# Kernel optimization log

Hardware: AMD Instinct MI355X
Metric: run time of the kernel (lower is better)

## Reference

```python
import jax, jax.numpy as jnp
import numpy as np

N_ITER = 2          # GenSP n_iter
M_COEF = 0.0        # GenSP M (positional-feature weight)
AFF_SOFTMAX = 1.0   # GenSP affinity_softmax


def setup_inputs() -> dict:
    key = jax.random.key(0)
    x = jax.random.normal(key, (2, 64, 256, 256), dtype=jnp.float32)
    return {"x": x, "stoken_size": 16}


def reference(x, stoken_size):
    # Faithful JAX version of GenSP.forward / ssn_iter (softmax_order='v0',
    # ws=None -> ws=2*stride0-1, i.e. each pixel searches its 9 neighboring
    # superpixel centroids; dist_type='l2' squared distance).
    B, C, H, W = x.shape
    s = int(stoken_size)
    nH, nW = (H - 1) // s + 1, (W - 1) // s + 1
    nS = nH * nW
    N = H * W

    # append_grid: concat scaled (y,x) coordinate channels, scale = M/stride0
    scale = jnp.asarray(M_COEF / s, x.dtype)
    gy, gx = jnp.meshgrid(jnp.arange(H, dtype=x.dtype) * scale,
                          jnp.arange(W, dtype=x.dtype) * scale, indexing='ij')
    grid = jnp.broadcast_to(jnp.stack([gy, gx])[None], (B, 2, H, W))
    feats = jnp.concatenate([x, grid], axis=1)          # [B, C+2, H, W]
    C2 = C + 2
    pf = feats.reshape(B, C2, N)                        # pixel features

    # calc_init_centroid: adaptive_avg_pool2d to (nH, nW); H,W divisible by s
    cent = feats.reshape(B, C2, nH, s, nW, s).mean(axis=(3, 5)).reshape(B, C2, nS)

    # per-pixel base superpixel cell and its 3x3 candidate neighborhood
    yy, xx = jnp.meshgrid(jnp.arange(H), jnp.arange(W), indexing='ij')
    sy = (yy // s).reshape(-1)                          # [N]
    sx = (xx // s).reshape(-1)
    dy, dx = jnp.meshgrid(jnp.arange(-1, 2), jnp.arange(-1, 2), indexing='ij')
    dy = dy.reshape(-1); dx = dx.reshape(-1)            # [9]
    cy = sy[:, None] + dy[None]                         # [N, 9]
    cx = sx[:, None] + dx[None]
    valid = (cy >= 0) & (cy < nH) & (cx >= 0) & (cx < nW)
    cand = jnp.where(valid, cy * nW + cx, 0)            # candidate spixel ids
    pix = jnp.broadcast_to(jnp.arange(N)[:, None], (N, 9))
    flat = (cand * N + pix).reshape(-1)                 # [9N] flat COO index
    NEG = jnp.asarray(-1e30, x.dtype)

    affinity = None
    for it in range(N_ITER):
        ck = cent[:, :, cand]                           # [B, C2, N, 9] gather
        d = jnp.sum((pf[:, :, :, None] - ck) ** 2, axis=1)  # squared-l2 [B,N,9]
        logits = jnp.where(valid[None], -AFF_SOFTMAX * d, NEG)
        w = jax.nn.softmax(logits, axis=-1)             # softmax_order 'v0'
        w = jnp.where(valid[None], w, jnp.asarray(0.0, x.dtype))
        # sparse-COO -> dense scatter: A[b, spix, pix] = w
        A = jnp.zeros((B, nS * N), x.dtype).at[:, flat].add(w.reshape(B, -1))
        affinity = A.reshape(B, nS, N)
        if it < N_ITER - 1:
            # spixel_features = bmm(A, pf^T) / (A.sum(2) + 1e-16)
            num = jnp.einsum('bsn,bcn->bcs', affinity, pf)
            den = affinity.sum(axis=2)[:, None] + 1e-16
            cent = num / den
    return affinity
```

## Files before the change

### kernel.cpp

```cpp
#include <hip/hip_runtime.h>
#include <cstdint>


__device__ __forceinline__ unsigned short f2bf(float f) {
    unsigned u = __float_as_uint(f);
    u = (u + 0x7FFFu + ((u >> 16) & 1u)) >> 16;
    return (unsigned short)u;
}
__device__ __forceinline__ float bf2f(unsigned short h) {
    return __uint_as_float(((unsigned)h) << 16);
}

__global__ __launch_bounds__(256) void kcent0(const float* __restrict__ x,
                                              float* __restrict__ cent0,
                                              float* __restrict__ numden) {
    __shared__ float red[64];
    int blk = blockIdx.x;
    int u = threadIdx.x;
    if (blk < 130) numden[blk * 256 + u] = 0.f;
    int b  = blk >> 10;
    int c  = (blk >> 4) & 63;
    int sy = blk & 15;
    const float4* s4 = (const float4*)(x + (((size_t)b << 22) | ((size_t)c << 16) | ((size_t)sy << 12)));
    float4 a0 = s4[u], a1 = s4[u + 256], a2 = s4[u + 512], a3 = s4[u + 768];
    float p = (a0.x + a0.y + a0.z + a0.w) + (a1.x + a1.y + a1.z + a1.w)
            + (a2.x + a2.y + a2.z + a2.w) + (a3.x + a3.y + a3.z + a3.w);
    p += __shfl_xor(p, 1, 64);
    p += __shfl_xor(p, 2, 64);
    int lane = u & 63, wv = u >> 6;
    if ((lane & 3) == 0) red[wv * 16 + (lane >> 2)] = p;
    __syncthreads();
    if (u < 16) {
        float v = (red[u] + red[16 + u] + red[32 + u] + red[48 + u]) * (1.0f / 256.0f);
        cent0[(((b << 8) | (sy << 4) | u) << 6) + c] = v;
    }
}

__global__ __launch_bounds__(256) void kiter0(const float* __restrict__ x,
                                              const float* __restrict__ cent0,
                                              float* __restrict__ num,
                                              float* __restrict__ den) {
    __shared__ __align__(16) float smem[12608];
    float* kc    = smem;
    float* w_lds = smem + 576;
    unsigned short* pS = (unsigned short*)(smem + 3648);
    float* part  = smem + 576;

    int blk = blockIdx.x;
    int b = blk >> 8, sidx = blk & 255;
    int sy = sidx >> 4, sx = sidx & 15;
    int t  = threadIdx.x;
    int py = t >> 4, px = t & 15;
    int n  = ((sy << 4) + py) * 256 + (sx << 4) + px;
    const float* xp = x + ((size_t)b << 22) + n;
    const float* cb = cent0 + ((size_t)b << 14);

    int candj[9]; bool valj[9];
#pragma unroll
    for (int j = 0; j < 9; j++) {
        int cy = sy + j / 3 - 1, cx = sx + j % 3 - 1;
        bool v = (cy >= 0) && (cy < 16) && (cx >= 0) && (cx < 16);
        valj[j] = v;
        candj[j] = v ? ((cy << 4) | cx) : 0;
    }

    for (int idx = t; idx < 576; idx += 256) {
        int j = idx >> 6, c = idx & 63;
        kc[idx] = cb[(candj[j] << 6) + c];
    }
    __syncthreads();

    float d[9];
#pragma unroll
    for (int j = 0; j < 9; j++) d[j] = 0.f;
#pragma unroll
    for (int c = 0; c < 64; c += 4) {
        float p0 = xp[(size_t)(c + 0) << 16];
        float p1 = xp[(size_t)(c + 1) << 16];
        float p2 = xp[(size_t)(c + 2) << 16];
        float p3 = xp[(size_t)(c + 3) << 16];
#pragma unroll
        for (int j = 0; j < 9; j++) {
            float4 k4 = *(const float4*)&kc[(j << 6) + c];
            float f0 = p0 - k4.x, f1 = p1 - k4.y, f2 = p2 - k4.z, f3 = p3 - k4.w;
            d[j] = fmaf(f0, f0, d[j]);
            d[j] = fmaf(f1, f1, d[j]);
            d[j] = fmaf(f2, f2, d[j]);
            d[j] = fmaf(f3, f3, d[j]);
        }
        *(ushort2*)&pS[t * 70 + c]     = make_ushort2(f2bf(p0), f2bf(p1));
        *(ushort2*)&pS[t * 70 + c + 2] = make_ushort2(f2bf(p2), f2bf(p3));
    }

    float M = -1e30f;
#pragma unroll
    for (int j = 0; j < 9; j++) if (valj[j]) M = fmaxf(M, -d[j]);
    float w[9], Z = 0.f;
#pragma unroll
    for (int j = 0; j < 9; j++) { w[j] = valj[j] ? __expf(-d[j] - M) : 0.f; Z += w[j]; }
    float rZ = 1.0f / Z;
#pragma unroll
    for (int j = 0; j < 9; j++) { w[j] *= rZ; w_lds[t * 12 + j] = w[j]; }

    __syncthreads();

    int tg = t >> 4, cg = t & 15;
    float acc[9][4];
    float dacc[9];
#pragma unroll
    for (int j = 0; j < 9; j++) {
        dacc[j] = 0.f;
        acc[j][0] = 0.f; acc[j][1] = 0.f; acc[j][2] = 0.f; acc[j][3] = 0.f;
    }
#pragma unroll 4
    for (int i = 0; i < 16; i++) {
        int tt = (tg << 4) + i;
        float4 wA = *(const float4*)&w_lds[tt * 12];
        float4 wB = *(const float4*)&w_lds[tt * 12 + 4];
        float  w8 = w_lds[tt * 12 + 8];
        ushort2 A2 = *(const ushort2*)&pS[tt * 70 + 4 * cg];
        ushort2 B2 = *(const ushort2*)&pS[tt * 70 + 4 * cg + 2];
        float p0 = bf2f(A2.x), p1 = bf2f(A2.y), p2v = bf2f(B2.x), p3v = bf2f(B2.y);
        float ww[9] = {wA.x, wA.y, wA.z, wA.w, wB.x, wB.y, wB.z, wB.w, w8};
#pragma unroll
        for (int j = 0; j < 9; j++) {
            dacc[j] += ww[j];
            acc[j][0] = fmaf(ww[j], p0, acc[j][0]);
            acc[j][1] = fmaf(ww[j], p1, acc[j][1]);
            acc[j][2] = fmaf(ww[j], p2v, acc[j][2]);
            acc[j][3] = fmaf(ww[j], p3v, acc[j][3]);
        }
    }

    __syncthreads();

#pragma unroll
    for (int j = 0; j < 9; j++)
        *(float4*)&part[tg * 592 + (j << 6) + (cg << 2)] =
            make_float4(acc[j][0], acc[j][1], acc[j][2], acc[j][3]);
    if (cg == 0) {
#pragma unroll
        for (int j = 0; j < 9; j++) part[tg * 592 + 576 + j] = dacc[j];
    }

    __syncthreads();

    for (int o = t; o < 585; o += 256) {
        float s = 0.f;
#pragma unroll
        for (int tg2 = 0; tg2 < 16; tg2++) s += part[tg2 * 592 + o];
        if (o < 576) {
            int j = o >> 6, c = o & 63;
            int cy = sy + j / 3 - 1, cx = sx + j % 3 - 1;
            if (cy >= 0 && cy < 16 && cx >= 0 && cx < 16)
                atomicAdd(&num[((size_t)((b << 8) | (cy << 4) | cx) << 6) + c], s);
        } else {
            int j = o - 576;
            int cy = sy + j / 3 - 1, cx = sx + j % 3 - 1;
            if (cy >= 0 && cy < 16 && cx >= 0 && cx < 16)
                atomicAdd(&den[(b << 8) | (cy << 4) | cx], s);
        }
    }
}

__global__ __launch_bounds__(256) void kdiv(const float* __restrict__ num,
                                            const float* __restrict__ den,
                                            float* __restrict__ cent1) {
    int i = blockIdx.x * 256 + threadIdx.x;
    cent1[i] = num[i] / (den[i >> 6] + 1e-16f);
}

__global__ __launch_bounds__(256) void kweights(const float* __restrict__ x,
                                                const float* __restrict__ cent1,
                                                float* __restrict__ W) {
    __shared__ __align__(16) float kc[576];
    int blk = blockIdx.x;
    int b = blk >> 8, sidx = blk & 255;
    int sy = sidx >> 4, sx = sidx & 15;
    int t  = threadIdx.x;
    int py = t >> 4, px = t & 15;
    int n  = ((sy << 4) + py) * 256 + (sx << 4) + px;
    const float* xp = x + ((size_t)b << 22) + n;
    const float* cb = cent1 + ((size_t)b << 14);

    int candj[9]; bool valj[9];
#pragma unroll
    for (int j = 0; j < 9; j++) {
        int cy = sy + j / 3 - 1, cx = sx + j % 3 - 1;
        bool v = (cy >= 0) && (cy < 16) && (cx >= 0) && (cx < 16);
        valj[j] = v;
        candj[j] = v ? ((cy << 4) | cx) : 0;
    }

    for (int idx = t; idx < 576; idx += 256) {
        int j = idx >> 6, c = idx & 63;
        kc[idx] = cb[(candj[j] << 6) + c];
    }
    __syncthreads();

    float d[9];
#pragma unroll
    for (int j = 0; j < 9; j++) d[j] = 0.f;
#pragma unroll
    for (int c = 0; c < 64; c += 4) {
        float p0 = xp[(size_t)(c + 0) << 16];
        float p1 = xp[(size_t)(c + 1) << 16];
        float p2 = xp[(size_t)(c + 2) << 16];
        float p3 = xp[(size_t)(c + 3) << 16];
#pragma unroll
        for (int j = 0; j < 9; j++) {
            float4 k4 = *(const float4*)&kc[(j << 6) + c];
            float f0 = p0 - k4.x, f1 = p1 - k4.y, f2 = p2 - k4.z, f3 = p3 - k4.w;
            d[j] = fmaf(f0, f0, d[j]);
            d[j] = fmaf(f1, f1, d[j]);
            d[j] = fmaf(f2, f2, d[j]);
            d[j] = fmaf(f3, f3, d[j]);
        }
    }

    float M = -1e30f;
#pragma unroll
    for (int j = 0; j < 9; j++) if (valj[j]) M = fmaxf(M, -d[j]);
    float w[9], Z = 0.f;
#pragma unroll
    for (int j = 0; j < 9; j++) { w[j] = valj[j] ? __expf(-d[j] - M) : 0.f; Z += w[j]; }
    float rZ = 1.0f / Z;

    float* wb = W + (((size_t)b * 9) << 16) + n;
#pragma unroll
    for (int j = 0; j < 9; j++)
        if (valj[j]) wb[(size_t)j << 16] = w[j] * rZ;
}

__global__ __launch_bounds__(256) void kexpand(const float4* __restrict__ W4,
                                               float4* __restrict__ out4) {
    unsigned g0 = blockIdx.x * 256u + threadIdx.x;
#pragma unroll
    for (int it = 0; it < 4; it++) {
        unsigned g = g0 + (unsigned)it * 2097152u;
        unsigned b = g >> 22;
        unsigned s = (g >> 14) & 255u;
        unsigned q = g & 16383u;
        int syn = (int)(q >> 10);
        int sxn = (int)((q >> 2) & 15u);
        int dy = (int)(s >> 4)  - syn;
        int dx = (int)(s & 15u) - sxn;
        float4 v = make_float4(0.f, 0.f, 0.f, 0.f);
        if (dy >= -1 && dy <= 1 && dx >= -1 && dx <= 1) {
            int j = (dy + 1) * 3 + (dx + 1);
            v = W4[(((size_t)b * 9 + j) << 14) + q];
        }
        out4[g] = v;
    }
}

extern "C" void kernel_launch(void* const* d_in, const int* in_sizes, int n_in,
                              void* d_out, int out_size, void* d_ws, size_t ws_size,
                              hipStream_t stream) {
    (void)in_sizes; (void)n_in; (void)out_size; (void)ws_size;
    const float* x = (const float*)d_in[0];
    float* out = (float*)d_out;
    float* ws  = (float*)d_ws;
    float* cent0 = ws;
    float* num   = ws + 32768;
    float* den   = ws + 65536;
    float* cent1 = ws + 66048;
    float* W     = ws + 98816;

    kcent0  <<<2048, 256, 0, stream>>>(x, cent0, num);
    kiter0  <<<512,  256, 0, stream>>>(x, cent0, num, den);
    kdiv    <<<128,  256, 0, stream>>>(num, den, cent1);
    kweights<<<512,  256, 0, stream>>>(x, cent1, W);
    kexpand <<<8192, 256, 0, stream>>>((const float4*)W, (float4*)out);
}
```

Baseline: 189.3 us.

## Expand squared distance into dot product and fuse centroid division into kweights

Rewrites the squared-L2 distance as 2·p·c − |c|² (dropping the per-pixel |p|² term, which cancels in the softmax), so the inner loop needs one FMA per channel per candidate instead of a subtract plus an FMA. Per-block centroid norms are computed by a few threads and staged in shared memory. The separate kdiv launch is removed: kweights now reads num and den directly and applies the reciprocal while loading its centroid tile. This trades some floating-point cancellation accuracy for fewer ALU operations and one fewer kernel launch.

```diff
diff --git a/kernel.cpp b/kernel.cpp
--- a/kernel.cpp
+++ b/kernel.cpp
@@ -40,11 +40,12 @@
                                               const float* __restrict__ cent0,
                                               float* __restrict__ num,
                                               float* __restrict__ den) {
-    __shared__ __align__(16) float smem[12608];
-    float* kc    = smem;
-    float* w_lds = smem + 576;
-    unsigned short* pS = (unsigned short*)(smem + 3648);
-    float* part  = smem + 576;
+    __shared__ __align__(16) float smem[12624];
+    float* kc     = smem;
+    float* cnormS = smem + 576;
+    float* w_lds  = smem + 592;
+    unsigned short* pS = (unsigned short*)(smem + 3664);
+    float* part   = smem + 592;
 
     int blk = blockIdx.x;
     int b = blk >> 8, sidx = blk & 255;
@@ -66,7 +67,13 @@
 
     for (int idx = t; idx < 576; idx += 256) {
         int j = idx >> 6, c = idx & 63;
-        kc[idx] = cb[(candj[j] << 6) + c];
+        kc[idx] = 2.0f * cb[(candj[j] << 6) + c];
+    }
+    if (t < 9) {
+        const float* cr = cb + (candj[t] << 6);
+        float cn = 0.f;
+        for (int c = 0; c < 64; c++) { float v = cr[c]; cn = fmaf(v, v, cn); }
+        cnormS[t] = cn;
     }
     __syncthreads();
 
@@ -82,22 +89,25 @@
 #pragma unroll
         for (int j = 0; j < 9; j++) {
             float4 k4 = *(const float4*)&kc[(j << 6) + c];
-            float f0 = p0 - k4.x, f1 = p1 - k4.y, f2 = p2 - k4.z, f3 = p3 - k4.w;
-            d[j] = fmaf(f0, f0, d[j]);
-            d[j] = fmaf(f1, f1, d[j]);
-            d[j] = fmaf(f2, f2, d[j]);
-            d[j] = fmaf(f3, f3, d[j]);
+            d[j] = fmaf(p0, k4.x, d[j]);
+            d[j] = fmaf(p1, k4.y, d[j]);
+            d[j] = fmaf(p2, k4.z, d[j]);
+            d[j] = fmaf(p3, k4.w, d[j]);
         }
         *(ushort2*)&pS[t * 70 + c]     = make_ushort2(f2bf(p0), f2bf(p1));
         *(ushort2*)&pS[t * 70 + c + 2] = make_ushort2(f2bf(p2), f2bf(p3));
     }
 
+    float l[9];
     float M = -1e30f;
 #pragma unroll
-    for (int j = 0; j < 9; j++) if (valj[j]) M = fmaxf(M, -d[j]);
+    for (int j = 0; j < 9; j++) {
+        l[j] = d[j] - cnormS[j];
+        if (valj[j]) M = fmaxf(M, l[j]);
+    }
     float w[9], Z = 0.f;
 #pragma unroll
-    for (int j = 0; j < 9; j++) { w[j] = valj[j] ? __expf(-d[j] - M) : 0.f; Z += w[j]; }
+    for (int j = 0; j < 9; j++) { w[j] = valj[j] ? __expf(l[j] - M) : 0.f; Z += w[j]; }
     float rZ = 1.0f / Z;
 #pragma unroll
     for (int j = 0; j < 9; j++) { w[j] *= rZ; w_lds[t * 12 + j] = w[j]; }
@@ -163,17 +173,15 @@
     }
 }
 
-__global__ __launch_bounds__(256) void kdiv(const float* __restrict__ num,
-                                            const float* __restrict__ den,
-                                            float* __restrict__ cent1) {
-    int i = blockIdx.x * 256 + threadIdx.x;
-    cent1[i] = num[i] / (den[i >> 6] + 1e-16f);
-}
-
 __global__ __launch_bounds__(256) void kweights(const float* __restrict__ x,
-                                                const float* __restrict__ cent1,
+                                                const float* __restrict__ num,
+                                                const float* __restrict__ den,
                                                 float* __restrict__ W) {
-    __shared__ __align__(16) float kc[576];
+    __shared__ __align__(16) float smem[608];
+    float* kc     = smem;
+    float* cnormS = smem + 576;
+    float* rdS    = smem + 592;
+
     int blk = blockIdx.x;
     int b = blk >> 8, sidx = blk & 255;
     int sy = sidx >> 4, sx = sidx & 15;
@@ -181,7 +189,8 @@
     int py = t >> 4, px = t & 15;
     int n  = ((sy << 4) + py) * 256 + (sx << 4) + px;
     const float* xp = x + ((size_t)b << 22) + n;
-    const float* cb = cent1 + ((size_t)b << 14);
+    const float* nb = num + ((size_t)b << 14);
+    const float* db = den + ((size_t)b << 8);
 
     int candj[9]; bool valj[9];
 #pragma unroll
@@ -192,9 +201,17 @@
         candj[j] = v ? ((cy << 4) | cx) : 0;
     }
 
+    if (t < 9) rdS[t] = 1.0f / (db[candj[t]] + 1e-16f);
+    __syncthreads();
     for (int idx = t; idx < 576; idx += 256) {
         int j = idx >> 6, c = idx & 63;
-        kc[idx] = cb[(candj[j] << 6) + c];
+        kc[idx] = 2.0f * nb[(candj[j] << 6) + c] * rdS[j];
+    }
+    if (t < 9) {
+        const float* nr = nb + (candj[t] << 6);
+        float rd = rdS[t], cn = 0.f;
+        for (int c = 0; c < 64; c++) { float v = nr[c] * rd; cn = fmaf(v, v, cn); }
+        cnormS[t] = cn;
     }
     __syncthreads();
 
@@ -210,20 +227,23 @@
 #pragma unroll
         for (int j = 0; j < 9; j++) {
             float4 k4 = *(const float4*)&kc[(j << 6) + c];
-            float f0 = p0 - k4.x, f1 = p1 - k4.y, f2 = p2 - k4.z, f3 = p3 - k4.w;
-            d[j] = fmaf(f0, f0, d[j]);
-            d[j] = fmaf(f1, f1, d[j]);
-            d[j] = fmaf(f2, f2, d[j]);
-            d[j] = fmaf(f3, f3, d[j]);
-        }
-    }
-
+            d[j] = fmaf(p0, k4.x, d[j]);
+            d[j] = fmaf(p1, k4.y, d[j]);
+            d[j] = fmaf(p2, k4.z, d[j]);
+            d[j] = fmaf(p3, k4.w, d[j]);
+        }
+    }
+
+    float l[9];
     float M = -1e30f;
 #pragma unroll
-    for (int j = 0; j < 9; j++) if (valj[j]) M = fmaxf(M, -d[j]);
+    for (int j = 0; j < 9; j++) {
+        l[j] = d[j] - cnormS[j];
+        if (valj[j]) M = fmaxf(M, l[j]);
+    }
     float w[9], Z = 0.f;
 #pragma unroll
-    for (int j = 0; j < 9; j++) { w[j] = valj[j] ? __expf(-d[j] - M) : 0.f; Z += w[j]; }
+    for (int j = 0; j < 9; j++) { w[j] = valj[j] ? __expf(l[j] - M) : 0.f; Z += w[j]; }
     float rZ = 1.0f / Z;
 
     float* wb = W + (((size_t)b * 9) << 16) + n;
@@ -264,12 +284,10 @@
     float* cent0 = ws;
     float* num   = ws + 32768;
     float* den   = ws + 65536;
-    float* cent1 = ws + 66048;
     float* W     = ws + 98816;
 
     kcent0  <<<2048, 256, 0, stream>>>(x, cent0, num);
     kiter0  <<<512,  256, 0, stream>>>(x, cent0, num, den);
-    kdiv    <<<128,  256, 0, stream>>>(num, den, cent1);
-    kweights<<<512,  256, 0, stream>>>(x, cent1, W);
+    kweights<<<512,  256, 0, stream>>>(x, num, den, W);
     kexpand <<<8192, 256, 0, stream>>>((const float4*)W, (float4*)out);
 }
```

Result: no change. 187.4 us (-1.0%).
